# Performance work log

Hardware: AMD Instinct MI355X
Metric: run time of the kernel (lower is better)

Reference implementation:

```python
import jax, jax.numpy as jnp
import numpy as np

N_NODES = 50000
N_EDGES = 625000
HIDDEN = 128
N_TYPES = 4


def setup_inputs() -> dict:
    key = jax.random.key(0)
    ks = jax.random.split(key, 10)
    s = 1.0 / np.sqrt(HIDDEN)
    return {
        "node_states": jax.random.normal(ks[0], (N_NODES, HIDDEN), dtype=jnp.float32),
        "edge_index": jax.random.randint(ks[1], (2, N_EDGES), 0, N_NODES, dtype=jnp.int64),
        "edge_type": jax.random.randint(ks[2], (N_EDGES,), 0, N_TYPES, dtype=jnp.int64),
        # per-edge-type Linear(hidden, hidden): weight [T, d, d] (torch: y = x @ W.T + b)
        "edge_W": jax.random.uniform(ks[3], (N_TYPES, HIDDEN, HIDDEN), jnp.float32, -s, s),
        "edge_b": jax.random.uniform(ks[4], (N_TYPES, HIDDEN), jnp.float32, -s, s),
        # GRUCell params (torch layout: [3d, d] for r|z|n gates)
        "w_ih": jax.random.uniform(ks[5], (3 * HIDDEN, HIDDEN), jnp.float32, -s, s),
        "w_hh": jax.random.uniform(ks[6], (3 * HIDDEN, HIDDEN), jnp.float32, -s, s),
        "b_ih": jax.random.uniform(ks[7], (3 * HIDDEN,), jnp.float32, -s, s),
        "b_hh": jax.random.uniform(ks[8], (3 * HIDDEN,), jnp.float32, -s, s),
    }


def reference(node_states, edge_index, edge_type, edge_W, edge_b, w_ih, w_hh, b_ih, b_hh):
    num_nodes = node_states.shape[0]
    src, dst = edge_index[0], edge_index[1]
    x_src = node_states[src]  # [E, d] gather of source states

    # per-edge-type linear; small fixed loop over edge types, masked accumulate
    msgs = jnp.zeros_like(x_src)
    for t in range(edge_W.shape[0]):
        m_t = x_src @ edge_W[t].T + edge_b[t]  # [E, d]
        msgs = msgs + jnp.where((edge_type == t)[:, None], m_t, 0.0)

    # scatter-sum messages into destination nodes
    agg = jax.ops.segment_sum(msgs, dst, num_segments=num_nodes)  # [N, d]

    # GRUCell(agg, node_states) — torch semantics
    gi = agg @ w_ih.T + b_ih          # [N, 3d]
    gh = node_states @ w_hh.T + b_hh  # [N, 3d]
    i_r, i_z, i_n = jnp.split(gi, 3, axis=1)
    h_r, h_z, h_n = jnp.split(gh, 3, axis=1)
    r = jax.nn.sigmoid(i_r + h_r)
    z = jax.nn.sigmoid(i_z + h_z)
    n = jnp.tanh(i_n + r * h_n)
    return (1.0 - z) * n + z * node_states
```

## Files before the change

kernel.cpp:

```cpp
#include <hip/hip_runtime.h>


typedef __attribute__((ext_vector_type(8))) short short8;
typedef __attribute__((ext_vector_type(4))) float floatx4;

#define HID 128
#define NTY 4
#define CAP 16
#define OVF_MAX 65536

__device__ __forceinline__ unsigned short f2bf(float f) {
    unsigned int u = __float_as_uint(f);
    unsigned int r = (u + 0x7fffu + ((u >> 16) & 1u)) >> 16;
    return (unsigned short)r;
}
__device__ __forceinline__ float bf2f(unsigned int lo16) {
    return __uint_as_float(lo16 << 16);
}
__device__ __forceinline__ float frcp(float x) { return __builtin_amdgcn_rcpf(x); }

__device__ __forceinline__ void gload16(const unsigned short* g, unsigned short* l) {
    __builtin_amdgcn_global_load_lds(
        (const __attribute__((address_space(1))) unsigned int*)g,
        (__attribute__((address_space(3))) unsigned int*)l,
        16, 0, 0);
}


__global__ void prep_fill_kernel(const float* __restrict__ h, unsigned short* __restrict__ hbf,
                                 const float* __restrict__ W, unsigned short* __restrict__ Wc,
                                 const float* __restrict__ w_ih, const float* __restrict__ w_hh,
                                 unsigned short* __restrict__ Wg, float* __restrict__ bias4,
                                 const float* __restrict__ b_ih, const float* __restrict__ b_hh,
                                 const int* __restrict__ src, const int* __restrict__ dst,
                                 const int* __restrict__ ety,
                                 int* __restrict__ cnti, int* __restrict__ csrF,
                                 int* __restrict__ ovfn, int2* __restrict__ ovf,
                                 int total4, int nb_cvt, int E) {
    int b = blockIdx.x, tt = threadIdx.x;
    if (b < nb_cvt) {
        int i = b * 256 + tt;
        if (i < total4) {
            float4 v = ((const float4*)h)[i];
            uint2 o;
            o.x = (unsigned int)f2bf(v.x) | ((unsigned int)f2bf(v.y) << 16);
            o.y = (unsigned int)f2bf(v.z) | ((unsigned int)f2bf(v.w) << 16);
            ((uint2*)hbf)[i] = o;
        }
    } else if (b < nb_cvt + 256) {
        int idx = (b - nb_cvt) * 256 + tt;
        int j = idx >> 9, rem = idx & 511;
        int t = rem >> 7, k = rem & 127;
        Wc[idx] = f2bf(W[(t * HID + j) * HID + k]);
    } else if (b < nb_cvt + 768) {
        int idx = (b - nb_cvt - 256) * 256 + tt;
        int row = idx >> 8, k = idx & 255;
        int j = row >> 2, g = row & 3;
        float v = 0.0f;
        if (g == 0) v = (k < 128) ? w_ih[j * 128 + k]         : w_hh[j * 128 + (k - 128)];
        else if (g == 1) v = (k < 128) ? w_ih[(128 + j) * 128 + k] : w_hh[(128 + j) * 128 + (k - 128)];
        else if (g == 2) v = (k < 128) ? w_ih[(256 + j) * 128 + k] : 0.0f;
        else             v = (k < 128) ? 0.0f : w_hh[(256 + j) * 128 + (k - 128)];
        Wg[idx] = f2bf(v);
    } else if (b == nb_cvt + 768) {
        if (tt < 128) {
            float4 v;
            v.x = b_ih[tt] + b_hh[tt];
            v.y = b_ih[128 + tt] + b_hh[128 + tt];
            v.z = b_ih[256 + tt];
            v.w = b_hh[256 + tt];
            ((float4*)bias4)[tt] = v;
        }
    } else {
        int e = (b - nb_cvt - 769) * 256 + tt;
        if (e < E) {
            int seg = dst[e] * 4 + ety[e];
            int pos = atomicAdd(&cnti[seg], 1);
            if (pos < CAP) {
                csrF[(size_t)seg * CAP + pos] = src[e];
            } else {
                int op = atomicAdd(ovfn, 1);
                if (op < OVF_MAX) ovf[op] = make_int2(seg, src[e]);
            }
        }
    }
}


__global__ void gather_fixed_kernel(const int* __restrict__ cnti, const int* __restrict__ csrF,
                                    const unsigned int* __restrict__ hbu,
                                    const int* __restrict__ ovfn, const int2* __restrict__ ovf,
                                    float4* __restrict__ cnt4f, unsigned int* __restrict__ Su, int N) {
    int w = blockIdx.x * (blockDim.x >> 6) + (threadIdx.x >> 6);
    if (w >= N) return;
    int lane = threadIdx.x & 63;

    int tot[4];
#pragma unroll
    for (int t = 0; t < 4; ++t)
        tot[t] = __builtin_amdgcn_readfirstlane(cnti[w * 4 + t]);

#pragma unroll 2
    for (int t = 0; t < 4; ++t) {
        int seg = w * 4 + t;
        int c = (tot[t] < CAP) ? tot[t] : CAP;
        int p[CAP];
        unsigned int u[CAP];
#pragma unroll
        for (int i = 0; i < CAP; ++i) if (i < c) p[i] = csrF[(size_t)seg * CAP + i];
#pragma unroll
        for (int i = 0; i < CAP; ++i) if (i < c) u[i] = hbu[(size_t)p[i] * 64 + lane];
        float s0 = 0.f, s1 = 0.f;
#pragma unroll
        for (int i = 0; i < CAP; ++i) {
            if (i < c) {
                s0 += bf2f(u[i] & 0xffffu);
                s1 += bf2f(u[i] >> 16);
            }
        }
        if (tot[t] > CAP) {
            int on = __builtin_amdgcn_readfirstlane(ovfn[0]);
            if (on > OVF_MAX) on = OVF_MAX;
            for (int k = 0; k < on; ++k) {
                int2 oe = ovf[k];
                if (oe.x == seg) {
                    unsigned int uu = hbu[(size_t)oe.y * 64 + lane];
                    s0 += bf2f(uu & 0xffffu);
                    s1 += bf2f(uu >> 16);
                }
            }
        }
        Su[(size_t)seg * 64 + lane] = (unsigned int)f2bf(s0) | ((unsigned int)f2bf(s1) << 16);
    }
    if (lane == 0)
        cnt4f[w] = make_float4((float)tot[0], (float)tot[1], (float)tot[2], (float)tot[3]);
}


__global__ __launch_bounds__(256, 3) void agg_gru(const unsigned short* __restrict__ S,
                                                  const unsigned short* __restrict__ Wc,
                                                  const unsigned short* __restrict__ Wg,
                                                  const unsigned short* __restrict__ hbf,
                                                  const float4* __restrict__ cnt4,
                                                  const float* __restrict__ eb,
                                                  const float4* __restrict__ bias4,
                                                  float* __restrict__ out, int M) {
    __shared__ __align__(16) unsigned char smem[49152];
    unsigned short* Sreg = (unsigned short*)smem;
    unsigned short* Hbt  = (unsigned short*)(smem + 8192);
    unsigned short* Wreg = (unsigned short*)(smem + 16384);
    unsigned short* Xag  = Sreg;
    float* OutsF = (float*)(smem + 16384);

    const int tid = threadIdx.x;
    const int m0 = blockIdx.x * 32;
    const int lane = tid & 63, w = tid >> 6;
    const int lm = lane & 15, quad = lane >> 4;

    floatx4 accA[2][2];
#pragma unroll
    for (int x = 0; x < 2; ++x)
#pragma unroll
        for (int y = 0; y < 2; ++y) accA[x][y] = (floatx4){0.f, 0.f, 0.f, 0.f};

#pragma unroll 1
    for (int c = 0; c < 4; ++c) {
#pragma unroll
        for (int i = 0; i < 2; ++i) {
            int k = w * 2 + i;
            int slot = k * 64 + lane;
            int row = slot >> 4, x = slot & 15;
            int grow = m0 + row; if (grow >= M) grow = M - 1;
            gload16(S + (size_t)grow * 512 + c * 128 + ((x ^ (row & 7)) << 3),
                    Sreg + k * 512);
        }
#pragma unroll
        for (int i = 0; i < 8; ++i) {
            int kk = w * 8 + i;
            int slot = kk * 64 + lane;
            int j = slot >> 4, x = slot & 15;
            gload16(Wc + (size_t)j * 512 + c * 128 + ((x ^ (j & 7)) << 3),
                    Wreg + kk * 512);
        }
        __syncthreads();
#pragma unroll
        for (int ss = 0; ss < 4; ++ss) {
            int g = ss * 4 + quad;
            short8 av[2], bw[2];
#pragma unroll
            for (int mi = 0; mi < 2; ++mi)
                av[mi] = *(const short8*)&Sreg[(mi * 16 + lm) * 128 + ((g ^ (lm & 7)) << 3)];
#pragma unroll
            for (int ni = 0; ni < 2; ++ni)
                bw[ni] = *(const short8*)&Wreg[(w * 32 + ni * 16 + lm) * 128 + ((g ^ (lm & 7)) << 3)];
#pragma unroll
            for (int mi = 0; mi < 2; ++mi)
#pragma unroll
                for (int ni = 0; ni < 2; ++ni)
                    accA[mi][ni] = __builtin_amdgcn_mfma_f32_16x16x32_bf16(av[mi], bw[ni], accA[mi][ni], 0, 0, 0);
        }
        __syncthreads();
    }

#pragma unroll
    for (int i = 0; i < 2; ++i) {
        int k = w * 2 + i;
        int slot = k * 64 + lane;
        int row = slot >> 4, x = slot & 15;
        int grow = m0 + row; if (grow >= M) grow = M - 1;
        gload16(hbf + (size_t)grow * HID + ((x ^ (row & 7)) << 3),
                Hbt + k * 512);
    }

    {
#pragma unroll
        for (int ni = 0; ni < 2; ++ni) {
            int j = w * 32 + ni * 16 + lm;
            float e0 = eb[j], e1 = eb[HID + j], e2 = eb[2 * HID + j], e3 = eb[3 * HID + j];
            int jg = j >> 3, jr = j & 7;
#pragma unroll
            for (int mi = 0; mi < 2; ++mi) {
#pragma unroll
                for (int r = 0; r < 4; ++r) {
                    int nl = mi * 16 + quad * 4 + r;
                    int gn = m0 + nl;
                    if (gn >= M) gn = M - 1;
                    float4 c4 = cnt4[gn];
                    float v = accA[mi][ni][r] + c4.x * e0 + c4.y * e1 + c4.z * e2 + c4.w * e3;
                    Xag[nl * 128 + ((jg ^ (nl & 7)) << 3) + jr] = f2bf(v);
                }
            }
        }
    }
    __syncthreads();

    float fin[4][2][2];

#pragma unroll 1
    for (int gc = 0; gc < 4; ++gc) {
        floatx4 acc2[2][2];
#pragma unroll
        for (int x = 0; x < 2; ++x)
#pragma unroll
            for (int y = 0; y < 2; ++y) acc2[x][y] = (floatx4){0.f, 0.f, 0.f, 0.f};

#pragma unroll 1
        for (int kc = 0; kc < 2; ++kc) {
#pragma unroll
            for (int i = 0; i < 8; ++i) {
                int kk = w * 8 + i;
                int slot = kk * 64 + lane;
                int rr = slot >> 4, x = slot & 15;
                gload16(Wg + (size_t)(gc * 128 + rr) * 256 + kc * 128 + ((x ^ (rr & 7)) << 3),
                        Wreg + kk * 512);
            }
            __syncthreads();
            const unsigned short* Bsrc = kc ? Hbt : Xag;
#pragma unroll
            for (int ss = 0; ss < 4; ++ss) {
                int g = ss * 4 + quad;
                short8 af[2], bfr[2];
#pragma unroll
                for (int mi2 = 0; mi2 < 2; ++mi2)
                    af[mi2] = *(const short8*)&Wreg[(w * 32 + mi2 * 16 + lm) * 128 + ((g ^ (lm & 7)) << 3)];
#pragma unroll
                for (int ni = 0; ni < 2; ++ni)
                    bfr[ni] = *(const short8*)&Bsrc[(ni * 16 + lm) * 128 + ((g ^ (lm & 7)) << 3)];
#pragma unroll
                for (int mi2 = 0; mi2 < 2; ++mi2)
#pragma unroll
                    for (int ni = 0; ni < 2; ++ni)
                        acc2[mi2][ni] = __builtin_amdgcn_mfma_f32_16x16x32_bf16(af[mi2], bfr[ni], acc2[mi2][ni], 0, 0, 0);
            }
            __syncthreads();
        }

#pragma unroll
        for (int mi2 = 0; mi2 < 2; ++mi2) {
            int j = gc * 32 + w * 8 + mi2 * 4 + quad;
            float4 bb = bias4[j];
            int jg = j >> 3, jr = j & 7;
#pragma unroll
            for (int ni = 0; ni < 2; ++ni) {
                int nl = ni * 16 + lm;
                float g0 = acc2[mi2][ni][0], g1 = acc2[mi2][ni][1];
                float g2 = acc2[mi2][ni][2], g3 = acc2[mi2][ni][3];
                float rr = frcp(1.f + __expf(-(g0 + bb.x)));
                float zz = frcp(1.f + __expf(-(g1 + bb.y)));
                float aa = g2 + bb.z + rr * (g3 + bb.w);
                float nn = 1.f - 2.f * frcp(1.f + __expf(2.f * aa));
                float hv = bf2f((unsigned int)Hbt[nl * 128 + ((jg ^ (nl & 7)) << 3) + jr]);
                fin[gc][mi2][ni] = nn + zz * (hv - nn);
            }
        }
    }
    __syncthreads();

#pragma unroll
    for (int gc = 0; gc < 4; ++gc) {
#pragma unroll
        for (int mi2 = 0; mi2 < 2; ++mi2) {
            int j = gc * 32 + w * 8 + mi2 * 4 + quad;
            int gq = j >> 2, jr = j & 3;
#pragma unroll
            for (int ni = 0; ni < 2; ++ni) {
                int nl = ni * 16 + lm;
                OutsF[nl * 128 + ((gq ^ (nl & 7)) << 2) + jr] = fin[gc][mi2][ni];
            }
        }
    }
    __syncthreads();

    {
        int row = tid >> 3;
        int cb = (tid & 7) * 16;
        int node = m0 + row;
        if (node < M) {
            float* dstp = out + (size_t)node * HID + cb;
#pragma unroll
            for (int i = 0; i < 4; ++i) {
                int gq = (cb >> 2) + i;
                *(float4*)(dstp + i * 4) = *(const float4*)&OutsF[row * 128 + ((gq ^ (row & 7)) << 2)];
            }
        }
    }
}


extern "C" void kernel_launch(void* const* d_in, const int* in_sizes, int n_in,
                              void* d_out, int out_size, void* d_ws, size_t ws_size,
                              hipStream_t stream) {
    const float* node_states = (const float*)d_in[0];
    const int*   edge_index  = (const int*)d_in[1];
    const int*   edge_type   = (const int*)d_in[2];
    const float* edge_W      = (const float*)d_in[3];
    const float* edge_b      = (const float*)d_in[4];
    const float* w_ih        = (const float*)d_in[5];
    const float* w_hh        = (const float*)d_in[6];
    const float* b_ih        = (const float*)d_in[7];
    const float* b_hh        = (const float*)d_in[8];

    const int M = in_sizes[0] / HID;
    const int E = in_sizes[1] / 2;
    const int N4 = M * 4;
    const int* src = edge_index;
    const int* dst = edge_index + E;

    char* ws = (char*)d_ws;
    size_t off = 0;
    unsigned short* hbf   = (unsigned short*)(ws + off); off += (size_t)M * HID * 2;
    float*          bias4 = (float*)(ws + off);          off += (size_t)128 * 4 * 4;
    unsigned short* S     = (unsigned short*)(ws + off); off += (size_t)M * 512 * 2;
    unsigned short* Wcat  = (unsigned short*)(ws + off); off += (size_t)128 * 512 * 2;
    unsigned short* Wgru  = (unsigned short*)(ws + off); off += (size_t)512 * 256 * 2;
    float*          cnt4f = (float*)(ws + off);          off += (size_t)M * 4 * 4;
    int*            cnti  = (int*)(ws + off);            off += (size_t)N4 * 4;
    int*            ovfn  = (int*)(ws + off);            off += 16;
    int2*           ovf   = (int2*)(ws + off);           off += (size_t)OVF_MAX * 8;
    int*            csrF  = (int*)(ws + off);            off += (size_t)N4 * CAP * 4;

    const int total4 = M * HID / 4;
    const int nb_cvt  = (total4 + 255) / 256;
    const int nb_fill = (E + 255) / 256;

    hipMemsetAsync(cnti, 0, (size_t)N4 * 4 + 16, stream);

    prep_fill_kernel<<<nb_cvt + 769 + nb_fill, 256, 0, stream>>>(
        node_states, hbf, edge_W, Wcat, w_ih, w_hh, Wgru, bias4, b_ih, b_hh,
        src, dst, edge_type, cnti, csrF, ovfn, ovf, total4, nb_cvt, E);

    gather_fixed_kernel<<<(M + 3) / 4, 256, 0, stream>>>(cnti, csrF, (const unsigned int*)hbf,
                                                         ovfn, ovf, (float4*)cnt4f,
                                                         (unsigned int*)S, M);

    agg_gru<<<(M + 31) / 32, 256, 0, stream>>>(S, Wcat, Wgru, hbf, (const float4*)cnt4f,
                                               edge_b, (const float4*)bias4, (float*)d_out, M);
}
```

Baseline: 234.9 us.

## Rebalance prep and gather kernels, move weight conversion into gather launch

The weight and bias bf16 conversion blocks move from the fill kernel into the gather kernel's launch. Each fill thread now converts two rows of node states or inserts two edges, with all edge loads issued before the atomics. The gather kernel gives each wave two edge types of one node instead of all four, which doubles the number of waves. CSR index loads become int4 vector loads. The aim is more memory-level parallelism and less serial work per wave, at the cost of more blocks and some extra branching.

Measured after the change: 245.0 us. +4.3%, slower.

```diff
diff --git a/kernel.cpp b/kernel.cpp
--- a/kernel.cpp
+++ b/kernel.cpp
@@ -28,10 +28,6 @@
 
 
 __global__ void prep_fill_kernel(const float* __restrict__ h, unsigned short* __restrict__ hbf,
-                                 const float* __restrict__ W, unsigned short* __restrict__ Wc,
-                                 const float* __restrict__ w_ih, const float* __restrict__ w_hh,
-                                 unsigned short* __restrict__ Wg, float* __restrict__ bias4,
-                                 const float* __restrict__ b_ih, const float* __restrict__ b_hh,
                                  const int* __restrict__ src, const int* __restrict__ dst,
                                  const int* __restrict__ ety,
                                  int* __restrict__ cnti, int* __restrict__ csrF,
@@ -39,21 +35,65 @@
                                  int total4, int nb_cvt, int E) {
     int b = blockIdx.x, tt = threadIdx.x;
     if (b < nb_cvt) {
-        int i = b * 256 + tt;
-        if (i < total4) {
-            float4 v = ((const float4*)h)[i];
-            uint2 o;
-            o.x = (unsigned int)f2bf(v.x) | ((unsigned int)f2bf(v.y) << 16);
-            o.y = (unsigned int)f2bf(v.z) | ((unsigned int)f2bf(v.w) << 16);
-            ((uint2*)hbf)[i] = o;
-        }
-    } else if (b < nb_cvt + 256) {
-        int idx = (b - nb_cvt) * 256 + tt;
+        int i0 = (b * 256 + tt) * 2;
+#pragma unroll
+        for (int k = 0; k < 2; ++k) {
+            int i = i0 + k;
+            if (i < total4) {
+                float4 v = ((const float4*)h)[i];
+                uint2 o;
+                o.x = (unsigned int)f2bf(v.x) | ((unsigned int)f2bf(v.y) << 16);
+                o.y = (unsigned int)f2bf(v.z) | ((unsigned int)f2bf(v.w) << 16);
+                ((uint2*)hbf)[i] = o;
+            }
+        }
+    } else {
+        int base = (b - nb_cvt) * 512;
+        int e0 = base + tt;
+        int e1 = base + 256 + tt;
+        int d0 = 0, t0 = 0, s0 = 0, d1 = 0, t1 = 0, s1 = 0;
+        bool v0 = e0 < E, v1 = e1 < E;
+        if (v0) { d0 = dst[e0]; t0 = ety[e0]; s0 = src[e0]; }
+        if (v1) { d1 = dst[e1]; t1 = ety[e1]; s1 = src[e1]; }
+        if (v0) {
+            int seg = d0 * 4 + t0;
+            int pos = atomicAdd(&cnti[seg], 1);
+            if (pos < CAP) csrF[(size_t)seg * CAP + pos] = s0;
+            else {
+                int op = atomicAdd(ovfn, 1);
+                if (op < OVF_MAX) ovf[op] = make_int2(seg, s0);
+            }
+        }
+        if (v1) {
+            int seg = d1 * 4 + t1;
+            int pos = atomicAdd(&cnti[seg], 1);
+            if (pos < CAP) csrF[(size_t)seg * CAP + pos] = s1;
+            else {
+                int op = atomicAdd(ovfn, 1);
+                if (op < OVF_MAX) ovf[op] = make_int2(seg, s1);
+            }
+        }
+    }
+}
+
+
+__global__ void gather_plus_kernel(const float* __restrict__ W, unsigned short* __restrict__ Wc,
+                                   const float* __restrict__ w_ih, const float* __restrict__ w_hh,
+                                   unsigned short* __restrict__ Wg, float* __restrict__ bias4,
+                                   const float* __restrict__ b_ih, const float* __restrict__ b_hh,
+                                   const int* __restrict__ cnti, const int* __restrict__ csrF,
+                                   const unsigned int* __restrict__ hbu,
+                                   const int* __restrict__ ovfn, const int2* __restrict__ ovf,
+                                   float* __restrict__ cnt2f, unsigned int* __restrict__ Su, int N) {
+    int b = blockIdx.x, tt = threadIdx.x;
+    if (b < 256) {
+        int idx = b * 256 + tt;
         int j = idx >> 9, rem = idx & 511;
         int t = rem >> 7, k = rem & 127;
         Wc[idx] = f2bf(W[(t * HID + j) * HID + k]);
-    } else if (b < nb_cvt + 768) {
-        int idx = (b - nb_cvt - 256) * 256 + tt;
+        return;
+    } else if (b < 768) {
+        int idx = (b - 256) * 256 + tt;
         int row = idx >> 8, k = idx & 255;
         int j = row >> 2, g = row & 3;
         float v = 0.0f;
@@ -62,7 +102,8 @@
         else if (g == 2) v = (k < 128) ? w_ih[(256 + j) * 128 + k] : 0.0f;
         else             v = (k < 128) ? 0.0f : w_hh[(256 + j) * 128 + (k - 128)];
         Wg[idx] = f2bf(v);
-    } else if (b == nb_cvt + 768) {
+        return;
+    } else if (b == 768) {
         if (tt < 128) {
             float4 v;
             v.x = b_ih[tt] + b_hh[tt];
@@ -71,43 +112,36 @@
             v.w = b_hh[256 + tt];
             ((float4*)bias4)[tt] = v;
         }
-    } else {
-        int e = (b - nb_cvt - 769) * 256 + tt;
-        if (e < E) {
-            int seg = dst[e] * 4 + ety[e];
-            int pos = atomicAdd(&cnti[seg], 1);
-            if (pos < CAP) {
-                csrF[(size_t)seg * CAP + pos] = src[e];
-            } else {
-                int op = atomicAdd(ovfn, 1);
-                if (op < OVF_MAX) ovf[op] = make_int2(seg, src[e]);
-            }
-        }
-    }
-}
-
-
-__global__ void gather_fixed_kernel(const int* __restrict__ cnti, const int* __restrict__ csrF,
-                                    const unsigned int* __restrict__ hbu,
-                                    const int* __restrict__ ovfn, const int2* __restrict__ ovf,
-                                    float4* __restrict__ cnt4f, unsigned int* __restrict__ Su, int N) {
-    int w = blockIdx.x * (blockDim.x >> 6) + (threadIdx.x >> 6);
-    if (w >= N) return;
-    int lane = threadIdx.x & 63;
-
-    int tot[4];
-#pragma unroll
-    for (int t = 0; t < 4; ++t)
-        tot[t] = __builtin_amdgcn_readfirstlane(cnti[w * 4 + t]);
-
-#pragma unroll 2
-    for (int t = 0; t < 4; ++t) {
-        int seg = w * 4 + t;
+        return;
+    }
+
+    int gb = b - 769;
+    int wv = tt >> 6;
+    int lane = tt & 63;
+    int node = gb * 2 + (wv >> 1);
+    if (node >= N) return;
+    int half = wv & 1;
+    int seg0 = node * 4 + half * 2;
+
+    int tot[2];
+    tot[0] = __builtin_amdgcn_readfirstlane(cnti[seg0]);
+    tot[1] = __builtin_amdgcn_readfirstlane(cnti[seg0 + 1]);
+
+#pragma unroll
+    for (int t = 0; t < 2; ++t) {
+        int seg = seg0 + t;
         int c = (tot[t] < CAP) ? tot[t] : CAP;
+        int4 pq[4];
+#pragma unroll
+        for (int q = 0; q < 4; ++q)
+            if (q * 4 < c) pq[q] = ((const int4*)csrF)[(size_t)seg * 4 + q];
         int p[CAP];
+#pragma unroll
+        for (int q = 0; q < 4; ++q) {
+            p[q * 4 + 0] = pq[q].x; p[q * 4 + 1] = pq[q].y;
+            p[q * 4 + 2] = pq[q].z; p[q * 4 + 3] = pq[q].w;
+        }
         unsigned int u[CAP];
-#pragma unroll
-        for (int i = 0; i < CAP; ++i) if (i < c) p[i] = csrF[(size_t)seg * CAP + i];
 #pragma unroll
         for (int i = 0; i < CAP; ++i) if (i < c) u[i] = hbu[(size_t)p[i] * 64 + lane];
         float s0 = 0.f, s1 = 0.f;
@@ -132,8 +166,9 @@
         }
         Su[(size_t)seg * 64 + lane] = (unsigned int)f2bf(s0) | ((unsigned int)f2bf(s1) << 16);
     }
-    if (lane == 0)
-        cnt4f[w] = make_float4((float)tot[0], (float)tot[1], (float)tot[2], (float)tot[3]);
+    if (lane == 0) {
+        ((float2*)cnt2f)[(size_t)node * 2 + half] = make_float2((float)tot[0], (float)tot[1]);
+    }
 }
 
 
@@ -360,18 +395,19 @@
     int*            csrF  = (int*)(ws + off);            off += (size_t)N4 * CAP * 4;
 
     const int total4 = M * HID / 4;
-    const int nb_cvt  = (total4 + 255) / 256;
-    const int nb_fill = (E + 255) / 256;
+    const int nb_cvt  = (total4 + 511) / 512;
+    const int nb_fill = (E + 511) / 512;
 
     hipMemsetAsync(cnti, 0, (size_t)N4 * 4 + 16, stream);
 
-    prep_fill_kernel<<<nb_cvt + 769 + nb_fill, 256, 0, stream>>>(
-        node_states, hbf, edge_W, Wcat, w_ih, w_hh, Wgru, bias4, b_ih, b_hh,
-        src, dst, edge_type, cnti, csrF, ovfn, ovf, total4, nb_cvt, E);
-
-    gather_fixed_kernel<<<(M + 3) / 4, 256, 0, stream>>>(cnti, csrF, (const unsigned int*)hbf,
-                                                         ovfn, ovf, (float4*)cnt4f,
-                                                         (unsigned int*)S, M);
+    prep_fill_kernel<<<nb_cvt + nb_fill, 256, 0, stream>>>(
+        node_states, hbf, src, dst, edge_type, cnti, csrF, ovfn, ovf,
+        total4, nb_cvt, E);
+
+    gather_plus_kernel<<<769 + (M + 1) / 2, 256, 0, stream>>>(
+        edge_W, Wcat, w_ih, w_hh, Wgru, bias4, b_ih, b_hh,
+        cnti, csrF, (const unsigned int*)hbf, ovfn, ovf,
+        cnt4f, (unsigned int*)S, M);
 
     agg_gru<<<(M + 31) / 32, 256, 0, stream>>>(S, Wcat, Wgru, hbf, (const float4*)cnt4f,
                                                edge_b, (const float4*)bias4, (float*)d_out, M);
```
